# Kernel optimization log

Measured on AMD Instinct MI355X. Metric: run time of the kernel, lower is better.

Reference implementation:

```python
import jax, jax.numpy as jnp
import numpy as np

H, B, D, C = 6, 512, 2048, 1000   # heads (5 ICs + backbone exit), batch, feat dim, classes
TAU = 0.5                          # confidence_threshold


def setup_inputs() -> dict:
    key = jax.random.key(0)
    k1, k2, k3, k4 = jax.random.split(key, 4)
    feats = jax.random.normal(k1, (H, B, D), dtype=jnp.float32)          # pooled reps at each exit
    W = jax.random.normal(k2, (H, D, C), dtype=jnp.float32) * 0.07       # per-head classifier weights
    b = jax.random.normal(k3, (H, C), dtype=jnp.float32) * 0.1
    y_true = jax.random.randint(k4, (B,), 0, C)
    return {"feats": feats, "W": W, "b": b, "y_true": y_true}


def reference(feats, W, b, y_true):
    # Per-head logits for every sample (vectorized replacement for the shrinking-batch loop).
    logits = jnp.einsum('hbd,hdc->hbc', feats, W) + b[:, None, :]        # [H, B, C]
    logp = jax.nn.log_softmax(logits, axis=-1)
    conf = jnp.exp(logp).max(axis=-1)                                    # [H, B] max softmax prob (prob_conf=True)

    # Early-exit routing: first head with conf >= TAU; else head with max confidence
    # (argmax returns the first occurrence, matching the strict '>' update in find_exit).
    exited = conf >= TAU                                                  # [H, B]
    any_exit = exited.any(axis=0)                                         # [B]
    first_exit = jnp.argmax(exited, axis=0)                               # [B] first True along heads
    best_conf = jnp.argmax(conf, axis=0)                                  # [B] fallback exit
    exit_idx = jnp.where(any_exit, first_exit, best_conf)                 # [B] == sample_exited_at

    # Gather the chosen head's logits per sample (vectorized masked-scatter of sample_outputs).
    outputs = jnp.take_along_axis(logits, exit_idx[None, :, None], axis=0)[0]   # [B, C]

    # criterion_ic: cross-entropy loss + accuracy on routed outputs
    out_logp = jax.nn.log_softmax(outputs, axis=-1)
    loss = -jnp.take_along_axis(out_logp, y_true[:, None], axis=1).mean()
    acc = (outputs.argmax(axis=-1) == y_true).astype(jnp.float32).mean()
    return outputs, exit_idx.astype(jnp.int32), loss, acc
```

## Files before the change

### kernel.cpp

```cpp
#include <hip/hip_runtime.h>
#include <hip/hip_bf16.h>
#include <math.h>

#define Hn 6
#define Bn 512
#define Dn 2048
#define Cn 1000
#define Cpad 1024
#define TAUv 0.5f
#define KSPLIT 2
#define KPER (Dn / KSPLIT)
#define NIT (KPER / 32)
#define NKT (Dn / 32)

typedef unsigned int u32;
typedef unsigned short u16;
typedef __attribute__((ext_vector_type(8))) short short8;
typedef __attribute__((ext_vector_type(4))) float f32x4;

union FragU { u32 d[4]; short8 s; };

__device__ __forceinline__ u32 cvt_pk2(float f0, float f1) {
  union { __hip_bfloat162 h; u32 u; } cv;
  cv.h = __float22bfloat162_rn(make_float2(f0, f1));
  return cv.u;
}

__device__ __forceinline__ void pack8(const float* rr, uint4& hv, uint4& lv) {
  u32 hd[4], ld[4];
  float r[8];
#pragma unroll
  for (int i = 0; i < 4; ++i) {
    const u32 d = cvt_pk2(rr[2 * i], rr[2 * i + 1]);
    hd[i] = d;
    r[2 * i]     = rr[2 * i]     - __uint_as_float(d << 16);
    r[2 * i + 1] = rr[2 * i + 1] - __uint_as_float(d & 0xffff0000u);
  }
#pragma unroll
  for (int i = 0; i < 4; ++i) ld[i] = cvt_pk2(r[2 * i], r[2 * i + 1]);
  hv = make_uint4(hd[0], hd[1], hd[2], hd[3]);
  lv = make_uint4(ld[0], ld[1], ld[2], ld[3]);
}

__device__ __forceinline__ void dma16(const void* g, void* l) {
  __builtin_amdgcn_global_load_lds(
      (const __attribute__((address_space(1))) u32*)g,
      (__attribute__((address_space(3))) u32*)l, 16, 0, 0);
}

__global__ __launch_bounds__(256) void conv_k(
    const float* __restrict__ feats, const float* __restrict__ W,
    u16* __restrict__ Ah, u16* __restrict__ Al,
    u16* __restrict__ Bh, u16* __restrict__ Bl)
{
  __shared__ float smem[128 * 33];
  const int t   = blockIdx.x;
  const int yy  = blockIdx.y;
  const int h   = blockIdx.z;
  const int tid = threadIdx.x;

  if (yy < 4) {
    const int r0 = yy * 128;
#pragma unroll
    for (int i = 0; i < 4; ++i) {
      const int f = i * 256 + tid;
      const int r = f >> 3, q = f & 7;
      const float4 v = *(const float4*)(feats + ((size_t)(h * Bn + r0 + r) * Dn + t * 32 + q * 4));
      smem[r * 33 + q * 4 + 0] = v.x; smem[r * 33 + q * 4 + 1] = v.y;
      smem[r * 33 + q * 4 + 2] = v.z; smem[r * 33 + q * 4 + 3] = v.w;
    }
    __syncthreads();
#pragma unroll
    for (int i = 0; i < 2; ++i) {
      const int j = i * 256 + tid;
      const int c = j >> 7, r = j & 127;
      float rr[8];
#pragma unroll
      for (int e = 0; e < 8; ++e) rr[e] = smem[r * 33 + c * 8 + e];
      uint4 hv, lv;
      pack8(rr, hv, lv);
      const size_t o = (((size_t)(h * 64 + t) * 4 + c) * 512 + r0 + r);
      ((uint4*)Ah)[o] = hv;
      ((uint4*)Al)[o] = lv;
    }
  } else {
    const int n0 = (yy - 4) * 128;
#pragma unroll
    for (int i = 0; i < 4; ++i) {
      const int f = i * 256 + tid;
      const int k = f >> 5, q = f & 31;
      const int n = n0 + q * 4;
      const float* src = W + ((size_t)h * Dn + t * 32 + k) * Cn;
      float4 v = make_float4(0.f, 0.f, 0.f, 0.f);
      if (n + 3 < Cn) {
        v = *(const float4*)(src + n);
      } else {
        if (n + 0 < Cn) v.x = src[n + 0];
        if (n + 1 < Cn) v.y = src[n + 1];
        if (n + 2 < Cn) v.z = src[n + 2];
        if (n + 3 < Cn) v.w = src[n + 3];
      }
      smem[k * 129 + q * 4 + 0] = v.x; smem[k * 129 + q * 4 + 1] = v.y;
      smem[k * 129 + q * 4 + 2] = v.z; smem[k * 129 + q * 4 + 3] = v.w;
    }
    __syncthreads();
#pragma unroll
    for (int i = 0; i < 2; ++i) {
      const int j = i * 256 + tid;
      const int c = j >> 7, n = j & 127;
      float rr[8];
#pragma unroll
      for (int e = 0; e < 8; ++e) rr[e] = smem[(c * 8 + e) * 129 + n];
      uint4 hv, lv;
      pack8(rr, hv, lv);
      const size_t o = (((size_t)(h * 64 + t) * 4 + c) * 1024 + n0 + n);
      ((uint4*)Bh)[o] = hv;
      ((uint4*)Bl)[o] = lv;
    }
  }
}

__global__ __launch_bounds__(256, 2) void gemm_k(
    const u16* __restrict__ AhG, const u16* __restrict__ AlG,
    const u16* __restrict__ BhG, const u16* __restrict__ BlG,
    const float* __restrict__ bias, float* __restrict__ logits)
{
  const int bid = blockIdx.x;
  const int wg = (bid & 7) * 48 + (bid >> 3);
  const int n0 = (wg & 7) * 128;
  const int m0 = ((wg >> 3) & 3) * 128;
  const int z  = wg >> 5;
  const int h  = z >> 1;
  const int kz = z & 1;
  const int t = threadIdx.x, lane = t & 63, w = t >> 6;

  __shared__ __align__(16) char lds[2][32768];

  const u16* gmat = (w == 0) ? AhG : (w == 1) ? AlG : (w == 2) ? BhG : BlG;
  const int  R    = (w < 2) ? 512 : 1024;
  const int  row0 = (w < 2) ? m0 : n0;
  const uint4* g0 = (const uint4*)gmat
                  + ((size_t)(h * 64 + kz * NIT) * 4) * R + row0 + lane;
  const int dstw = w * 8192 + lane * 16;

  const int fl = lane & 15, fq = lane >> 4;
  const int wm = (w & 1) * 64, wn = (w >> 1) * 64;

  f32x4 acc[4][4];
#pragma unroll
  for (int i = 0; i < 4; ++i)
#pragma unroll
    for (int j = 0; j < 4; ++j) acc[i][j] = (f32x4){0.f, 0.f, 0.f, 0.f};

#define STAGE(TILE)                                                                   \
  {                                                                                   \
    char* sb = &lds[(TILE) & 1][0];                                                   \
    const uint4* g = g0 + (size_t)(TILE) * 4 * R;                                     \
    _Pragma("unroll")                                                                 \
    for (int i = 0; i < 8; ++i)                                                       \
      dma16(g + (size_t)(i >> 1) * R + (i & 1) * 64, sb + dstw + i * 1024);           \
  }

#define COMPUTE_TILE(IT)                                                              \
  {                                                                                   \
    const char* bb = &lds[(IT) & 1][0];                                               \
    FragU ah[4], al[4];                                                               \
    _Pragma("unroll")                                                                 \
    for (int mt = 0; mt < 4; ++mt) {                                                  \
      const int r = wm + mt * 16 + fl;                                                \
      ah[mt].s = *(const short8*)(bb + (fq * 128 + r) * 16);                          \
      al[mt].s = *(const short8*)(bb + 8192 + (fq * 128 + r) * 16);                   \
    }                                                                                 \
    _Pragma("unroll")                                                                 \
    for (int nt = 0; nt < 4; ++nt) {                                                  \
      const int n = wn + nt * 16 + fl;                                                \
      FragU bh, bl;                                                                   \
      bh.s = *(const short8*)(bb + 16384 + (fq * 128 + n) * 16);                      \
      bl.s = *(const short8*)(bb + 24576 + (fq * 128 + n) * 16);                      \
      _Pragma("unroll")                                                               \
      for (int mt = 0; mt < 4; ++mt) {                                                \
        acc[mt][nt] = __builtin_amdgcn_mfma_f32_16x16x32_bf16(ah[mt].s, bh.s, acc[mt][nt], 0, 0, 0); \
        acc[mt][nt] = __builtin_amdgcn_mfma_f32_16x16x32_bf16(ah[mt].s, bl.s, acc[mt][nt], 0, 0, 0); \
        acc[mt][nt] = __builtin_amdgcn_mfma_f32_16x16x32_bf16(al[mt].s, bh.s, acc[mt][nt], 0, 0, 0); \
      }                                                                               \
    }                                                                                 \
  }

  STAGE(0);

  for (int it = 0; it < NIT - 1; ++it) {
    STAGE(it + 1);
    asm volatile("s_waitcnt vmcnt(8)" ::: "memory");
    __builtin_amdgcn_s_barrier();
    __builtin_amdgcn_sched_barrier(0);
    __builtin_amdgcn_s_setprio(1);
    COMPUTE_TILE(it);
    __builtin_amdgcn_s_setprio(0);
    __builtin_amdgcn_sched_barrier(0);
    asm volatile("s_waitcnt lgkmcnt(0)" ::: "memory");
    __builtin_amdgcn_s_barrier();
  }
  asm volatile("s_waitcnt vmcnt(0)" ::: "memory");
  __builtin_amdgcn_s_barrier();
  __builtin_amdgcn_sched_barrier(0);
  __builtin_amdgcn_s_setprio(1);
  COMPUTE_TILE(NIT - 1);
  __builtin_amdgcn_s_setprio(0);
#undef COMPUTE_TILE
#undef STAGE

  float* part = logits + (size_t)kz * ((size_t)Hn * Bn * Cn);
#pragma unroll
  for (int nt = 0; nt < 4; ++nt) {
    const int col = n0 + wn + nt * 16 + fl;
    if (col >= Cn) continue;
    const float bv = (kz == 0) ? bias[(size_t)h * Cn + col] : 0.f;
#pragma unroll
    for (int mt = 0; mt < 4; ++mt) {
      const int rbase = m0 + wm + mt * 16 + fq * 4;
#pragma unroll
      for (int r = 0; r < 4; ++r)
        part[((size_t)h * Bn + rbase + r) * Cn + col] = acc[mt][nt][r] + bv;
    }
  }
}

__global__ __launch_bounds__(256) void confpick_k(
    const float* __restrict__ logits, const int* __restrict__ y,
    float* __restrict__ out, float* __restrict__ out_exit,
    float* __restrict__ loss_b, float* __restrict__ corr_b)
{
  const int b = blockIdx.x, tid = threadIdx.x;
  const int lane = tid & 63, w = tid >> 6;
  const size_t S = (size_t)Hn * Bn * Cn;
  __shared__ float ms[Hn], ss[Hn];

  for (int h = w; h < Hn; h += 4) {
    const float* p = logits + ((size_t)h * Bn + b) * Cn;
    float vv[16];
#pragma unroll
    for (int i = 0; i < 4; ++i) {
      const int c4 = i * 256 + lane * 4;
      if (c4 + 3 < Cn) {
        const float4 v0 = *(const float4*)(p + c4);
        const float4 v1 = *(const float4*)(p + S + c4);
        vv[4 * i + 0] = v0.x + v1.x;
        vv[4 * i + 1] = v0.y + v1.y;
        vv[4 * i + 2] = v0.z + v1.z;
        vv[4 * i + 3] = v0.w + v1.w;
      } else {
#pragma unroll
        for (int j = 0; j < 4; ++j) {
          const int c = c4 + j;
          vv[4 * i + j] = (c < Cn) ? p[c] + p[S + c] : -3.4e38f;
        }
      }
    }
    float m = -3.4e38f;
#pragma unroll
    for (int i = 0; i < 16; ++i) m = fmaxf(m, vv[i]);
#pragma unroll
    for (int off = 32; off >= 1; off >>= 1) m = fmaxf(m, __shfl_xor(m, off));
    float s = 0.f;
#pragma unroll
    for (int i = 0; i < 16; ++i) s += (vv[i] > -3.0e38f) ? expf(vv[i] - m) : 0.f;
#pragma unroll
    for (int off = 32; off >= 1; off >>= 1) s += __shfl_xor(s, off);
    if (lane == 0) { ms[h] = m; ss[h] = s; }
  }
  __syncthreads();

  int first = -1, best = 0;
  float bestc = -3.4e38f;
#pragma unroll
  for (int h = 0; h < Hn; ++h) {
    const float c = 1.0f / ss[h];
    if (first < 0 && c >= TAUv) first = h;
    if (c > bestc) { bestc = c; best = h; }
  }
  const int ex = (first >= 0) ? first : best;
  const float* p = logits + ((size_t)ex * Bn + b) * Cn;

  const int c4 = tid * 4;
  float vv[4] = {-3.4e38f, -3.4e38f, -3.4e38f, -3.4e38f};
  if (c4 + 3 < Cn) {
    const float4 v0 = *(const float4*)(p + c4);
    const float4 v1 = *(const float4*)(p + S + c4);
    vv[0] = v0.x + v1.x;
    vv[1] = v0.y + v1.y;
    vv[2] = v0.z + v1.z;
    vv[3] = v0.w + v1.w;
  }
  float vm = -3.4e38f; int im = 1 << 30;
#pragma unroll
  for (int j = 0; j < 4; ++j) {
    const int c = c4 + j;
    if (c < Cn) {
      out[(size_t)b * Cn + c] = vv[j];
      if (vv[j] > vm) { vm = vv[j]; im = c; }
    }
  }
#pragma unroll
  for (int off = 32; off >= 1; off >>= 1) {
    const float ov = __shfl_xor(vm, off);
    const int   oi = __shfl_xor(im, off);
    if (ov > vm || (ov == vm && oi < im)) { vm = ov; im = oi; }
  }
  __shared__ float rm[4]; __shared__ int ri[4];
  if (lane == 0) { rm[w] = vm; ri[w] = im; }
  __syncthreads();
  if (tid == 0) {
    float bm = rm[0]; int bi = ri[0];
    for (int q = 1; q < 4; ++q)
      if (rm[q] > bm || (rm[q] == bm && ri[q] < bi)) { bm = rm[q]; bi = ri[q]; }
    const int yt = y[b];
    const float ryt = p[yt] + p[S + yt];
    const float lp = ryt - ms[ex] - logf(ss[ex]);
    out_exit[b] = (float)ex;
    loss_b[b] = -lp;
    corr_b[b] = (bi == yt) ? 1.f : 0.f;
  }
}

__global__ __launch_bounds__(256) void reduce_k(
    const float* __restrict__ loss_b, const float* __restrict__ corr_b,
    float* __restrict__ scalars)
{
  const int t = threadIdx.x, lane = t & 63, w = t >> 6;
  float l = loss_b[t] + loss_b[t + 256];
  float c = corr_b[t] + corr_b[t + 256];
#pragma unroll
  for (int off = 32; off >= 1; off >>= 1) {
    l += __shfl_xor(l, off);
    c += __shfl_xor(c, off);
  }
  __shared__ float sl[4], sc[4];
  if (lane == 0) { sl[w] = l; sc[w] = c; }
  __syncthreads();
  if (t == 0) {
    scalars[0] = (sl[0] + sl[1] + sl[2] + sl[3]) * (1.0f / (float)Bn);
    scalars[1] = (sc[0] + sc[1] + sc[2] + sc[3]) * (1.0f / (float)Bn);
  }
}

extern "C" void kernel_launch(void* const* d_in, const int* in_sizes, int n_in,
                              void* d_out, int out_size, void* d_ws, size_t ws_size,
                              hipStream_t stream) {
  const float* feats = (const float*)d_in[0];
  const float* W     = (const float*)d_in[1];
  const float* bias  = (const float*)d_in[2];
  const int*   y     = (const int*)d_in[3];
  float* out = (float*)d_out;

  float* logits = (float*)d_ws;
  float* loss_b = logits + (size_t)KSPLIT * Hn * Bn * Cn;
  float* corr_b = loss_b + Bn;
  u16*   AhG    = (u16*)(corr_b + Bn + 64);
  u16*   AlG    = AhG + (size_t)Hn * NKT * 4 * 512 * 8;
  u16*   BhG    = AlG + (size_t)Hn * NKT * 4 * 512 * 8;
  u16*   BlG    = BhG + (size_t)Hn * NKT * 4 * 1024 * 8;
  float* out_exit    = out + (size_t)Bn * Cn;
  float* out_scalars = out + (size_t)Bn * Cn + Bn;

  conv_k<<<dim3(NKT, 12, Hn), 256, 0, stream>>>(feats, W, AhG, AlG, BhG, BlG);
  gemm_k<<<dim3(384, 1, 1), 256, 0, stream>>>(AhG, AlG, BhG, BlG, bias, logits);
  confpick_k<<<Bn, 256, 0, stream>>>(logits, y, out, out_exit, loss_b, corr_b);
  reduce_k<<<1, 256, 0, stream>>>(loss_b, corr_b, out_scalars);
}
```

Baseline: 169.8 us.

## Drop split-K, use 64x64 GEMM tiles with triple buffering, fuse final reduce

The GEMM no longer splits K across two partial outputs. It now uses 64x64 output tiles over 768 workgroups with a three-stage LDS pipeline and three blocks per CU. This removes the second partial-logits buffer, its write traffic and the extra reads in the confidence/pick kernel. The final scalar reduction moves into the pick kernel through an atomic ticket (last-block pattern), which removes one kernel launch. The cost is less data reuse per tile, since smaller tiles mean more global reloads of A and B, and each block now runs a full-length K loop.

```diff
diff --git a/kernel.cpp b/kernel.cpp
--- a/kernel.cpp
+++ b/kernel.cpp
@@ -8,9 +8,7 @@
 #define Cn 1000
 #define Cpad 1024
 #define TAUv 0.5f
-#define KSPLIT 2
-#define KPER (Dn / KSPLIT)
-#define NIT (KPER / 32)
+#define NITF 64
 #define NKT (Dn / 32)
 
 typedef unsigned int u32;
@@ -51,13 +49,15 @@
 __global__ __launch_bounds__(256) void conv_k(
     const float* __restrict__ feats, const float* __restrict__ W,
     u16* __restrict__ Ah, u16* __restrict__ Al,
-    u16* __restrict__ Bh, u16* __restrict__ Bl)
+    u16* __restrict__ Bh, u16* __restrict__ Bl, u32* __restrict__ ticket)
 {
   __shared__ float smem[128 * 33];
   const int t   = blockIdx.x;
   const int yy  = blockIdx.y;
   const int h   = blockIdx.z;
   const int tid = threadIdx.x;
+
+  if (t == 0 && yy == 0 && h == 0 && tid == 0) *ticket = 0;
 
   if (yy < 4) {
     const int r0 = yy * 128;
@@ -120,65 +120,62 @@
   }
 }
 
-__global__ __launch_bounds__(256, 2) void gemm_k(
+__global__ __launch_bounds__(256, 3) void gemm_k(
     const u16* __restrict__ AhG, const u16* __restrict__ AlG,
     const u16* __restrict__ BhG, const u16* __restrict__ BlG,
     const float* __restrict__ bias, float* __restrict__ logits)
 {
   const int bid = blockIdx.x;
-  const int wg = (bid & 7) * 48 + (bid >> 3);
-  const int n0 = (wg & 7) * 128;
-  const int m0 = ((wg >> 3) & 3) * 128;
-  const int z  = wg >> 5;
-  const int h  = z >> 1;
-  const int kz = z & 1;
+  const int wg = (bid & 7) * 96 + (bid >> 3);
+  const int n0 = (wg & 15) * 64;
+  const int m0 = ((wg >> 4) & 7) * 64;
+  const int h  = wg >> 7;
   const int t = threadIdx.x, lane = t & 63, w = t >> 6;
 
-  __shared__ __align__(16) char lds[2][32768];
+  __shared__ __align__(16) char lds[3][16384];
 
   const u16* gmat = (w == 0) ? AhG : (w == 1) ? AlG : (w == 2) ? BhG : BlG;
   const int  R    = (w < 2) ? 512 : 1024;
   const int  row0 = (w < 2) ? m0 : n0;
-  const uint4* g0 = (const uint4*)gmat
-                  + ((size_t)(h * 64 + kz * NIT) * 4) * R + row0 + lane;
-  const int dstw = w * 8192 + lane * 16;
+  const uint4* g0 = (const uint4*)gmat + ((size_t)(h * 64) * 4) * R + row0 + lane;
+  const int dstw = w * 4096 + lane * 16;
 
   const int fl = lane & 15, fq = lane >> 4;
-  const int wm = (w & 1) * 64, wn = (w >> 1) * 64;
-
-  f32x4 acc[4][4];
-#pragma unroll
-  for (int i = 0; i < 4; ++i)
-#pragma unroll
-    for (int j = 0; j < 4; ++j) acc[i][j] = (f32x4){0.f, 0.f, 0.f, 0.f};
-
-#define STAGE(TILE)                                                                   \
+  const int wm = (w & 1) * 32, wn = (w >> 1) * 32;
+
+  f32x4 acc[2][2];
+#pragma unroll
+  for (int i = 0; i < 2; ++i)
+#pragma unroll
+    for (int j = 0; j < 2; ++j) acc[i][j] = (f32x4){0.f, 0.f, 0.f, 0.f};
+
+#define STAGE(TILE, BUF)                                                              \
   {                                                                                   \
-    char* sb = &lds[(TILE) & 1][0];                                                   \
+    char* sb = &lds[BUF][0];                                                          \
     const uint4* g = g0 + (size_t)(TILE) * 4 * R;                                     \
     _Pragma("unroll")                                                                 \
-    for (int i = 0; i < 8; ++i)                                                       \
-      dma16(g + (size_t)(i >> 1) * R + (i & 1) * 64, sb + dstw + i * 1024);           \
-  }
-
-#define COMPUTE_TILE(IT)                                                              \
+    for (int c = 0; c < 4; ++c)                                                       \
+      dma16(g + (size_t)c * R, sb + dstw + c * 1024);                                 \
+  }
+
+#define COMPUTE_TILE(BUF)                                                             \
   {                                                                                   \
-    const char* bb = &lds[(IT) & 1][0];                                               \
-    FragU ah[4], al[4];                                                               \
+    const char* bb = &lds[BUF][0];                                                    \
+    FragU ah[2], al[2];                                                               \
     _Pragma("unroll")                                                                 \
-    for (int mt = 0; mt < 4; ++mt) {                                                  \
+    for (int mt = 0; mt < 2; ++mt) {                                                  \
       const int r = wm + mt * 16 + fl;                                                \
-      ah[mt].s = *(const short8*)(bb + (fq * 128 + r) * 16);                          \
-      al[mt].s = *(const short8*)(bb + 8192 + (fq * 128 + r) * 16);                   \
+      ah[mt].s = *(const short8*)(bb + (fq * 64 + r) * 16);                           \
+      al[mt].s = *(const short8*)(bb + 4096 + (fq * 64 + r) * 16);                    \
     }                                                                                 \
     _Pragma("unroll")                                                                 \
-    for (int nt = 0; nt < 4; ++nt) {                                                  \
+    for (int nt = 0; nt < 2; ++nt) {                                                  \
       const int n = wn + nt * 16 + fl;                                                \
       FragU bh, bl;                                                                   \
-      bh.s = *(const short8*)(bb + 16384 + (fq * 128 + n) * 16);                      \
-      bl.s = *(const short8*)(bb + 24576 + (fq * 128 + n) * 16);                      \
+      bh.s = *(const short8*)(bb + 8192  + (fq * 64 + n) * 16);                       \
+      bl.s = *(const short8*)(bb + 12288 + (fq * 64 + n) * 16);                       \
       _Pragma("unroll")                                                               \
-      for (int mt = 0; mt < 4; ++mt) {                                                \
+      for (int mt = 0; mt < 2; ++mt) {                                                \
         acc[mt][nt] = __builtin_amdgcn_mfma_f32_16x16x32_bf16(ah[mt].s, bh.s, acc[mt][nt], 0, 0, 0); \
         acc[mt][nt] = __builtin_amdgcn_mfma_f32_16x16x32_bf16(ah[mt].s, bl.s, acc[mt][nt], 0, 0, 0); \
         acc[mt][nt] = __builtin_amdgcn_mfma_f32_16x16x32_bf16(al[mt].s, bh.s, acc[mt][nt], 0, 0, 0); \
@@ -186,41 +183,45 @@
     }                                                                                 \
   }
 
-  STAGE(0);
-
-  for (int it = 0; it < NIT - 1; ++it) {
-    STAGE(it + 1);
-    asm volatile("s_waitcnt vmcnt(8)" ::: "memory");
+  STAGE(0, 0);
+  STAGE(1, 1);
+
+  int bc = 0;
+  for (int it = 0; it < NITF; ++it) {
+    if (it + 2 < NITF) {
+      const int pb = (bc + 2 >= 3) ? (bc - 1) : (bc + 2);
+      STAGE(it + 2, pb);
+    }
+    if (it < NITF - 2)
+      asm volatile("s_waitcnt vmcnt(8)" ::: "memory");
+    else if (it == NITF - 2)
+      asm volatile("s_waitcnt vmcnt(4)" ::: "memory");
+    else
+      asm volatile("s_waitcnt vmcnt(0)" ::: "memory");
     __builtin_amdgcn_s_barrier();
     __builtin_amdgcn_sched_barrier(0);
     __builtin_amdgcn_s_setprio(1);
-    COMPUTE_TILE(it);
+    COMPUTE_TILE(bc);
     __builtin_amdgcn_s_setprio(0);
     __builtin_amdgcn_sched_barrier(0);
     asm volatile("s_waitcnt lgkmcnt(0)" ::: "memory");
     __builtin_amdgcn_s_barrier();
-  }
-  asm volatile("s_waitcnt vmcnt(0)" ::: "memory");
-  __builtin_amdgcn_s_barrier();
-  __builtin_amdgcn_sched_barrier(0);
-  __builtin_amdgcn_s_setprio(1);
-  COMPUTE_TILE(NIT - 1);
-  __builtin_amdgcn_s_setprio(0);
+    bc = (bc + 1 >= 3) ? 0 : bc + 1;
+  }
 #undef COMPUTE_TILE
 #undef STAGE
 
-  float* part = logits + (size_t)kz * ((size_t)Hn * Bn * Cn);
-#pragma unroll
-  for (int nt = 0; nt < 4; ++nt) {
+#pragma unroll
+  for (int nt = 0; nt < 2; ++nt) {
     const int col = n0 + wn + nt * 16 + fl;
     if (col >= Cn) continue;
-    const float bv = (kz == 0) ? bias[(size_t)h * Cn + col] : 0.f;
-#pragma unroll
-    for (int mt = 0; mt < 4; ++mt) {
+    const float bv = bias[(size_t)h * Cn + col];
+#pragma unroll
+    for (int mt = 0; mt < 2; ++mt) {
       const int rbase = m0 + wm + mt * 16 + fq * 4;
 #pragma unroll
       for (int r = 0; r < 4; ++r)
-        part[((size_t)h * Bn + rbase + r) * Cn + col] = acc[mt][nt][r] + bv;
+        logits[((size_t)h * Bn + rbase + r) * Cn + col] = acc[mt][nt][r] + bv;
     }
   }
 }
@@ -228,11 +229,11 @@
 __global__ __launch_bounds__(256) void confpick_k(
     const float* __restrict__ logits, const int* __restrict__ y,
     float* __restrict__ out, float* __restrict__ out_exit,
-    float* __restrict__ loss_b, float* __restrict__ corr_b)
+    float* __restrict__ loss_b, float* __restrict__ corr_b,
+    u32* __restrict__ ticket, float* __restrict__ scalars)
 {
   const int b = blockIdx.x, tid = threadIdx.x;
   const int lane = tid & 63, w = tid >> 6;
-  const size_t S = (size_t)Hn * Bn * Cn;
   __shared__ float ms[Hn], ss[Hn];
 
   for (int h = w; h < Hn; h += 4) {
@@ -243,16 +244,13 @@
       const int c4 = i * 256 + lane * 4;
       if (c4 + 3 < Cn) {
         const float4 v0 = *(const float4*)(p + c4);
-        const float4 v1 = *(const float4*)(p + S + c4);
-        vv[4 * i + 0] = v0.x + v1.x;
-        vv[4 * i + 1] = v0.y + v1.y;
-        vv[4 * i + 2] = v0.z + v1.z;
-        vv[4 * i + 3] = v0.w + v1.w;
+        vv[4 * i + 0] = v0.x; vv[4 * i + 1] = v0.y;
+        vv[4 * i + 2] = v0.z; vv[4 * i + 3] = v0.w;
       } else {
 #pragma unroll
         for (int j = 0; j < 4; ++j) {
           const int c = c4 + j;
-          vv[4 * i + j] = (c < Cn) ? p[c] + p[S + c] : -3.4e38f;
+          vv[4 * i + j] = (c < Cn) ? p[c] : -3.4e38f;
         }
       }
     }
@@ -285,11 +283,7 @@
   float vv[4] = {-3.4e38f, -3.4e38f, -3.4e38f, -3.4e38f};
   if (c4 + 3 < Cn) {
     const float4 v0 = *(const float4*)(p + c4);
-    const float4 v1 = *(const float4*)(p + S + c4);
-    vv[0] = v0.x + v1.x;
-    vv[1] = v0.y + v1.y;
-    vv[2] = v0.z + v1.z;
-    vv[3] = v0.w + v1.w;
+    vv[0] = v0.x; vv[1] = v0.y; vv[2] = v0.z; vv[3] = v0.w;
   }
   float vm = -3.4e38f; int im = 1 << 30;
 #pragma unroll
@@ -307,6 +301,7 @@
     if (ov > vm || (ov == vm && oi < im)) { vm = ov; im = oi; }
   }
   __shared__ float rm[4]; __shared__ int ri[4];
+  __shared__ u32 tk;
   if (lane == 0) { rm[w] = vm; ri[w] = im; }
   __syncthreads();
   if (tid == 0) {
@@ -314,32 +309,31 @@
     for (int q = 1; q < 4; ++q)
       if (rm[q] > bm || (rm[q] == bm && ri[q] < bi)) { bm = rm[q]; bi = ri[q]; }
     const int yt = y[b];
-    const float ryt = p[yt] + p[S + yt];
-    const float lp = ryt - ms[ex] - logf(ss[ex]);
+    const float lp = p[yt] - ms[ex] - logf(ss[ex]);
     out_exit[b] = (float)ex;
     loss_b[b] = -lp;
     corr_b[b] = (bi == yt) ? 1.f : 0.f;
-  }
-}
-
-__global__ __launch_bounds__(256) void reduce_k(
-    const float* __restrict__ loss_b, const float* __restrict__ corr_b,
-    float* __restrict__ scalars)
-{
-  const int t = threadIdx.x, lane = t & 63, w = t >> 6;
-  float l = loss_b[t] + loss_b[t + 256];
-  float c = corr_b[t] + corr_b[t + 256];
-#pragma unroll
-  for (int off = 32; off >= 1; off >>= 1) {
-    l += __shfl_xor(l, off);
-    c += __shfl_xor(c, off);
-  }
-  __shared__ float sl[4], sc[4];
-  if (lane == 0) { sl[w] = l; sc[w] = c; }
+    __threadfence();
+    tk = atomicAdd(ticket, 1u);
+  }
   __syncthreads();
-  if (t == 0) {
-    scalars[0] = (sl[0] + sl[1] + sl[2] + sl[3]) * (1.0f / (float)Bn);
-    scalars[1] = (sc[0] + sc[1] + sc[2] + sc[3]) * (1.0f / (float)Bn);
+
+  if (tk == (u32)(Bn - 1)) {
+    __threadfence();
+    float l = loss_b[tid] + loss_b[tid + 256];
+    float c = corr_b[tid] + corr_b[tid + 256];
+#pragma unroll
+    for (int off = 32; off >= 1; off >>= 1) {
+      l += __shfl_xor(l, off);
+      c += __shfl_xor(c, off);
+    }
+    __shared__ float sl[4], sc[4];
+    if (lane == 0) { sl[w] = l; sc[w] = c; }
+    __syncthreads();
+    if (tid == 0) {
+      scalars[0] = (sl[0] + sl[1] + sl[2] + sl[3]) * (1.0f / (float)Bn);
+      scalars[1] = (sc[0] + sc[1] + sc[2] + sc[3]) * (1.0f / (float)Bn);
+    }
   }
 }
 
@@ -353,17 +347,18 @@
   float* out = (float*)d_out;
 
   float* logits = (float*)d_ws;
-  float* loss_b = logits + (size_t)KSPLIT * Hn * Bn * Cn;
+  float* loss_b = logits + (size_t)Hn * Bn * Cn;
   float* corr_b = loss_b + Bn;
-  u16*   AhG    = (u16*)(corr_b + Bn + 64);
+  u32*   ticket = (u32*)(corr_b + Bn);
+  u16*   AhG    = (u16*)(ticket + 64);
   u16*   AlG    = AhG + (size_t)Hn * NKT * 4 * 512 * 8;
   u16*   BhG    = AlG + (size_t)Hn * NKT * 4 * 512 * 8;
   u16*   BlG    = BhG + (size_t)Hn * NKT * 4 * 1024 * 8;
   float* out_exit    = out + (size_t)Bn * Cn;
   float* out_scalars = out + (size_t)Bn * Cn + Bn;
 
-  conv_k<<<dim3(NKT, 12, Hn), 256, 0, stream>>>(feats, W, AhG, AlG, BhG, BlG);
-  gemm_k<<<dim3(384, 1, 1), 256, 0, stream>>>(AhG, AlG, BhG, BlG, bias, logits);
-  confpick_k<<<Bn, 256, 0, stream>>>(logits, y, out, out_exit, loss_b, corr_b);
-  reduce_k<<<1, 256, 0, stream>>>(loss_b, corr_b, out_scalars);
-}
+  conv_k<<<dim3(NKT, 12, Hn), 256, 0, stream>>>(feats, W, AhG, AlG, BhG, BlG, ticket);
+  gemm_k<<<dim3(768, 1, 1), 256, 0, stream>>>(AhG, AlG, BhG, BlG, bias, logits);
+  confpick_k<<<Bn, 256, 0, stream>>>(logits, y, out, out_exit, loss_b, corr_b,
+                                     ticket, out_scalars);
+}
```

New measurement: 175.1 us. +3.1%, slower.
